# Kernel optimization log

Measured on AMD Instinct MI355X. Metric: run time of the kernel, lower is better.

Reference implementation:

```python
import jax, jax.numpy as jnp
import numpy as np

B, T, H, V, IN = 128, 1024, 512, 256, 1

def _uniform(key, shape, fan):
    bound = 1.0 / np.sqrt(fan)
    return jax.random.uniform(key, shape, jnp.float32, -bound, bound)

def setup_inputs() -> dict:
    key = jax.random.key(0)
    ks = jax.random.split(key, 11)
    return {
        'x': jax.random.normal(ks[0], (B, T), jnp.float32),
        # PyTorch LSTMCell params: weight_ih [4H, in], weight_hh [4H, H], biases [4H]
        'W_ih1': _uniform(ks[1], (4 * H, IN), H),
        'W_hh1': _uniform(ks[2], (4 * H, H), H),
        'b_ih1': _uniform(ks[3], (4 * H,), H),
        'b_hh1': _uniform(ks[4], (4 * H,), H),
        'W_ih2': _uniform(ks[5], (4 * H, H), H),
        'W_hh2': _uniform(ks[6], (4 * H, H), H),
        'b_ih2': _uniform(ks[7], (4 * H,), H),
        'b_hh2': _uniform(ks[8], (4 * H,), H),
        'W_lin': _uniform(ks[9], (V, H), H),
        'b_lin': _uniform(ks[10], (V,), H),
    }

def _lstm_cell(x, h, c, W_ih, W_hh, b_ih, b_hh):
    # gates in PyTorch order: input, forget, cell(g), output
    g = x @ W_ih.T + b_ih + h @ W_hh.T + b_hh  # [B, 4H]
    i, f, gg, o = jnp.split(g, 4, axis=-1)
    c_new = jax.nn.sigmoid(f) * c + jax.nn.sigmoid(i) * jnp.tanh(gg)
    h_new = jax.nn.sigmoid(o) * jnp.tanh(c_new)
    return h_new, c_new

def reference(x, W_ih1, W_hh1, b_ih1, b_hh1, W_ih2, W_hh2, b_ih2, b_hh2, W_lin, b_lin):
    Bb, Tt = x.shape
    Hh = W_hh1.shape[1]
    xt = x.T[:, :, None]  # [T, B, 1] -- each timestep is a [B,1] chunk

    def step(carry, x_t):
        h1, c1, h2, c2 = carry
        h1, c1 = _lstm_cell(x_t, h1, c1, W_ih1, W_hh1, b_ih1, b_hh1)
        h2, c2 = _lstm_cell(h1, h2, c2, W_ih2, W_hh2, b_ih2, b_hh2)
        return (h1, c1, h2, c2), h2

    z = jnp.zeros((Bb, Hh), x.dtype)
    _, h2_all = jax.lax.scan(step, (z, z, z, z), xt)  # h2_all: [T, B, H]
    # per-step linear + softmax is time-independent -> batch it after the scan
    logits = jnp.einsum('tbh,vh->btv', h2_all, W_lin) + b_lin  # [B, T, V]
    return jax.nn.softmax(logits, axis=-1)
```

## Files before the change

### kernel.cpp

```cpp
#include <hip/hip_runtime.h>
#include <hip/hip_bf16.h>

#define BB 128
#define TT 1024
#define HH 512
#define VV 256
#define NBLK 128

typedef __attribute__((ext_vector_type(8))) short short8;
typedef __attribute__((ext_vector_type(4))) float floatx4;

__device__ __forceinline__ floatx4 mfma16(short8 a, short8 b, floatx4 c) {
    return __builtin_amdgcn_mfma_f32_16x16x32_bf16(a, b, c, 0, 0, 0);
}
__device__ __forceinline__ float sigm(float x) { return 1.0f / (1.0f + __expf(-x)); }
__device__ __forceinline__ float tanh_fast(float x) {
    return 2.0f / (1.0f + __expf(-2.0f * x)) - 1.0f;
}
__device__ __forceinline__ void vmcnt0() {
    asm volatile("s_waitcnt vmcnt(0)" ::: "memory");
}
__device__ __forceinline__ void vm_fence() {
    asm volatile("s_waitcnt vmcnt(0)" ::: "memory");
    __builtin_amdgcn_sched_barrier(0);
}
__device__ __forceinline__ unsigned ald32(const unsigned* p) {
    return __hip_atomic_load(p, __ATOMIC_RELAXED, __HIP_MEMORY_SCOPE_AGENT);
}
__device__ __forceinline__ void ast32(unsigned* p, unsigned v) {
    __hip_atomic_store(p, v, __ATOMIC_RELAXED, __HIP_MEMORY_SCOPE_AGENT);
}
__device__ __forceinline__ short8 ld16_sc1(const __hip_bfloat16* p) {
    short8 v;
    asm volatile("global_load_dwordx4 %0, %1, off sc1" : "=v"(v) : "v"(p));
    return v;
}

__device__ __forceinline__ void poll1(const unsigned* line, unsigned tgt, int lane) {
    for (;;) {
        unsigned v = tgt;
        if (lane < 32) v = ald32(line + lane);
        if (__all((int)(v >= tgt))) return;
        __builtin_amdgcn_s_sleep(1);
    }
}
__device__ __forceinline__ void poll2(const unsigned* lineA, unsigned tA,
                                      const unsigned* lineB, unsigned tB, int lane) {
    const unsigned* p = (lane < 32) ? (lineA + lane) : (lineB + (lane - 32));
    const unsigned tgt = (lane < 32) ? tA : tB;
    for (;;) {
        unsigned v = ald32(p);
        if (__all((int)(v >= tgt))) return;
        __builtin_amdgcn_s_sleep(1);
    }
}

__global__ __launch_bounds__(256) void canon(
    const float* __restrict__ x,
    const float* __restrict__ Whh1, const float* __restrict__ Wih2,
    const float* __restrict__ Whh2, const float* __restrict__ Wlin,
    const float* __restrict__ bih1, const float* __restrict__ bhh1,
    const float* __restrict__ bih2, const float* __restrict__ bhh2,
    __hip_bfloat16* __restrict__ Whh1c, __hip_bfloat16* __restrict__ Wih2c,
    __hip_bfloat16* __restrict__ Whh2c, __hip_bfloat16* __restrict__ Wlinc,
    float* __restrict__ bsum1, float* __restrict__ bsum2,
    float* __restrict__ xT)
{
    const int tid = blockIdx.x * 256 + threadIdx.x;
    const int np  = gridDim.x * 256;
    for (int i = tid; i < 2048 * 512; i += np) {
        Whh1c[i] = __float2bfloat16(Whh1[i]);
        Wih2c[i] = __float2bfloat16(Wih2[i]);
        Whh2c[i] = __float2bfloat16(Whh2[i]);
    }
    for (int i = tid; i < 256 * 512; i += np) Wlinc[i] = __float2bfloat16(Wlin[i]);
    for (int i = tid; i < 2048; i += np) {
        bsum1[i] = bih1[i] + bhh1[i];
        bsum2[i] = bih2[i] + bhh2[i];
    }
    for (int i = tid; i < BB * TT; i += np) {
        int b = i >> 10, t = i & 1023;
        xT[t * BB + b] = x[i];
    }
}

__global__ __launch_bounds__(256, 1) void lstm_persist(
    const float* __restrict__ xT,
    const float* __restrict__ Wih1,
    const __hip_bfloat16* __restrict__ Whh1c,
    const float* __restrict__ bsum1,
    const __hip_bfloat16* __restrict__ Wih2c,
    const __hip_bfloat16* __restrict__ Whh2c,
    const float* __restrict__ bsum2,
    unsigned* __restrict__ flags,
    unsigned* __restrict__ h2ring,
    unsigned* __restrict__ h1all,
    __hip_bfloat16* __restrict__ h2slots)
{
    extern __shared__ __hip_bfloat16 lds[];

    const int bid   = blockIdx.x;
    const int stage = bid >> 6;
    const int half  = (bid >> 5) & 1;
    const int lb    = bid & 31;
    const int j0    = lb * 16;
    const int b0    = half * 64;
    const int w     = threadIdx.x >> 6;
    const int lane  = threadIdx.x & 63;
    const int q     = lane >> 4, ln = lane & 15;
    const int r0    = b0 + w * 16;

    unsigned* myflag       = flags + (stage * 2 + half) * 1024 + lb;
    const unsigned* line1  = flags + half * 1024;
    const unsigned* line2  = flags + (2 + half) * 1024;

    {
        const __hip_bfloat16* S0 = (stage == 0) ? Whh1c : Wih2c;
        for (int idx = threadIdx.x; idx < 4096; idx += 256) {
            const int g = idx >> 10, kk = (idx >> 6) & 15, l = idx & 63;
            const int lnt = l & 15, qt = l >> 4;
            const size_t src = (size_t)(g * 512 + j0 + lnt) * 512 + kk * 32 + qt * 8;
            *(float4*)(lds + idx * 8) = *(const float4*)(S0 + src);
            if (stage == 1)
                *(float4*)(lds + 32768 + idx * 8) = *(const float4*)(Whh2c + src);
        }
    }
    __syncthreads();

    float wv[4], bs[4];
    #pragma unroll
    for (int g = 0; g < 4; ++g) {
        const int j = g * 512 + j0 + ln;
        if (stage == 0) { wv[g] = Wih1[j]; bs[g] = bsum1[j]; }
        else            { wv[g] = 0.0f;    bs[g] = bsum2[j]; }
    }
    float cre[4] = {0.0f, 0.0f, 0.0f, 0.0f};

    const __hip_bfloat16* h1bf = (const __hip_bfloat16*)h1all;
    const int aoff = (r0 + ln) * HH + q * 8;
    const int jc   = j0 + (ln & ~1);
    const int rA   = (ln & 1) ? 2 : 0;
    const int bA   = r0 + q * 4 + rA;

    for (int t = 0; t < TT; ++t) {
        floatx4 acc[4];
        #pragma unroll
        for (int g = 0; g < 4; ++g) acc[g] = floatx4{0, 0, 0, 0};
        unsigned pk[4];

        if (stage == 0) {
            if (w == 0 && t > 0) poll1(line1, (unsigned)t, lane);
            __syncthreads();
            const __hip_bfloat16* hA = h1bf + (size_t)t * 65536;
            float4 xv4 = *(const float4*)(xT + t * BB + r0 + q * 4);
            short8 A0[16];
            #pragma unroll
            for (int kk = 0; kk < 16; ++kk)
                A0[kk] = *(const short8*)(hA + aoff + kk * 32);
            #pragma unroll
            for (int kk = 0; kk < 16; ++kk) {
                #pragma unroll
                for (int g = 0; g < 4; ++g)
                    acc[g] = mfma16(A0[kk],
                        *(const short8*)(lds + ((g * 16 + kk) * 64 + lane) * 8), acc[g]);
            }
            #pragma unroll
            for (int reg = 0; reg < 4; ++reg) {
                const float xv = ((const float*)&xv4)[reg];
                float gi = acc[0][reg] + xv * wv[0] + bs[0];
                float gf = acc[1][reg] + xv * wv[1] + bs[1];
                float gg = acc[2][reg] + xv * wv[2] + bs[2];
                float go = acc[3][reg] + xv * wv[3] + bs[3];
                float cn = sigm(gf) * cre[reg] + sigm(gi) * tanh_fast(gg);
                cre[reg] = cn;
                float hn = sigm(go) * tanh_fast(cn);
                __hip_bfloat16 hb = __float2bfloat16(hn);
                unsigned short us; __builtin_memcpy(&us, &hb, 2);
                unsigned mine = us;
                unsigned other = (unsigned)__shfl_xor((int)mine, 1, 64);
                pk[reg] = (ln & 1) ? ((other & 0xffffu) | (mine << 16))
                                   : ((mine & 0xffffu) | (other << 16));
            }
            unsigned* dst = h1all + (size_t)(t + 1) * 32768;
            ast32(dst + ((bA * HH + jc) >> 1),       pk[rA]);
            ast32(dst + (((bA + 1) * HH + jc) >> 1), pk[rA + 1]);
        } else {
            if (w == 0) poll2(line1, (unsigned)(t + 1), line2, (unsigned)t, lane);
            __syncthreads();
            const __hip_bfloat16* hB =
                (const __hip_bfloat16*)h2ring + (size_t)(t & 3) * 65536;
            short8 A1[16];
            #pragma unroll
            for (int kk = 0; kk < 16; ++kk) A1[kk] = ld16_sc1(hB + aoff + kk * 32);
            const __hip_bfloat16* hA = h1bf + (size_t)(t + 1) * 65536;
            short8 A0[16];
            #pragma unroll
            for (int kk = 0; kk < 16; ++kk)
                A0[kk] = *(const short8*)(hA + aoff + kk * 32);
            vm_fence();
            #pragma unroll
            for (int kk = 0; kk < 16; ++kk) {
                #pragma unroll
                for (int g = 0; g < 4; ++g)
                    acc[g] = mfma16(A0[kk],
                        *(const short8*)(lds + ((g * 16 + kk) * 64 + lane) * 8), acc[g]);
            }
            #pragma unroll
            for (int kk = 0; kk < 16; ++kk) {
                #pragma unroll
                for (int g = 0; g < 4; ++g)
                    acc[g] = mfma16(A1[kk],
                        *(const short8*)(lds + 32768 + ((g * 16 + kk) * 64 + lane) * 8), acc[g]);
            }
            #pragma unroll
            for (int reg = 0; reg < 4; ++reg) {
                float gi = acc[0][reg] + bs[0];
                float gf = acc[1][reg] + bs[1];
                float gg = acc[2][reg] + bs[2];
                float go = acc[3][reg] + bs[3];
                float cn = sigm(gf) * cre[reg] + sigm(gi) * tanh_fast(gg);
                cre[reg] = cn;
                float hn = sigm(go) * tanh_fast(cn);
                __hip_bfloat16 hb = __float2bfloat16(hn);
                unsigned short us; __builtin_memcpy(&us, &hb, 2);
                unsigned mine = us;
                unsigned other = (unsigned)__shfl_xor((int)mine, 1, 64);
                pk[reg] = (ln & 1) ? ((other & 0xffffu) | (mine << 16))
                                   : ((mine & 0xffffu) | (other << 16));
            }
            unsigned* dst = h2ring + (size_t)((t + 1) & 3) * 32768;
            ast32(dst + ((bA * HH + jc) >> 1),       pk[rA]);
            ast32(dst + (((bA + 1) * HH + jc) >> 1), pk[rA + 1]);
            unsigned* outs = (unsigned*)h2slots;
            outs[(((size_t)bA * TT + t) * HH + jc) >> 1]       = pk[rA];
            outs[(((size_t)(bA + 1) * TT + t) * HH + jc) >> 1] = pk[rA + 1];
        }

        vmcnt0();
        __syncthreads();
        if (threadIdx.x == 0) ast32(myflag, (unsigned)(t + 1));
    }
}

__global__ __launch_bounds__(256) void lin_softmax(
    const __hip_bfloat16* __restrict__ Wlinc,
    const float* __restrict__ blin,
    float* out)
{
    const __hip_bfloat16* slots = (const __hip_bfloat16*)out;
    const int w = threadIdx.x >> 6;
    const int lane = threadIdx.x & 63;
    const int q = lane >> 4, ln = lane & 15;
    const int r0 = blockIdx.x * 64 + w * 16;

    floatx4 acc[16];
    #pragma unroll
    for (int n = 0; n < 16; ++n) acc[n] = floatx4{0, 0, 0, 0};

    const size_t arow = (size_t)(r0 + ln) * HH + q * 8;
    #pragma unroll 4
    for (int kk = 0; kk < 16; ++kk) {
        short8 a = *(const short8*)(slots + arow + kk * 32);
        #pragma unroll
        for (int n = 0; n < 16; ++n) {
            short8 bf = *(const short8*)(Wlinc + (n * 16 + ln) * HH + kk * 32 + q * 8);
            acc[n] = mfma16(a, bf, acc[n]);
        }
    }

    float bl[16];
    #pragma unroll
    for (int n = 0; n < 16; ++n) bl[n] = blin[n * 16 + ln];

    #pragma unroll
    for (int reg = 0; reg < 4; ++reg) {
        float v[16];
        float mx = -3.4e38f;
        #pragma unroll
        for (int n = 0; n < 16; ++n) {
            v[n] = acc[n][reg] + bl[n];
            mx = fmaxf(mx, v[n]);
        }
        #pragma unroll
        for (int m = 1; m < 16; m <<= 1) mx = fmaxf(mx, __shfl_xor(mx, m));
        float sum = 0.0f;
        #pragma unroll
        for (int n = 0; n < 16; ++n) { v[n] = __expf(v[n] - mx); sum += v[n]; }
        #pragma unroll
        for (int m = 1; m < 16; m <<= 1) sum += __shfl_xor(sum, m);
        const float inv = 1.0f / sum;

        const int r = r0 + q * 4 + reg;
        #pragma unroll
        for (int n = 0; n < 16; ++n)
            out[(size_t)r * VV + n * 16 + ln] = v[n] * inv;
    }
}

extern "C" void kernel_launch(void* const* d_in, const int* in_sizes, int n_in,
                              void* d_out, int out_size, void* d_ws, size_t ws_size,
                              hipStream_t stream)
{
    const float* x     = (const float*)d_in[0];
    const float* W_ih1 = (const float*)d_in[1];
    const float* W_hh1 = (const float*)d_in[2];
    const float* b_ih1 = (const float*)d_in[3];
    const float* b_hh1 = (const float*)d_in[4];
    const float* W_ih2 = (const float*)d_in[5];
    const float* W_hh2 = (const float*)d_in[6];
    const float* b_ih2 = (const float*)d_in[7];
    const float* b_hh2 = (const float*)d_in[8];
    const float* W_lin = (const float*)d_in[9];
    const float* b_lin = (const float*)d_in[10];

    char* p = (char*)d_ws;
    unsigned* flags  = (unsigned*)p;   p += 16384;
    unsigned* h2ring = (unsigned*)p;   p += (size_t)4 * 131072;
    unsigned* h1all  = (unsigned*)p;   p += (size_t)1025 * 131072;
    const size_t zbytes = 16384 + (size_t)4 * 131072 + 131072;
    float* bsum1 = (float*)p;          p += 2048 * 4;
    float* bsum2 = (float*)p;          p += 2048 * 4;
    float* xT    = (float*)p;          p += (size_t)BB * TT * 4;
    __hip_bfloat16* Whh1c = (__hip_bfloat16*)p; p += (size_t)2048 * 512 * 2;
    __hip_bfloat16* Wih2c = (__hip_bfloat16*)p; p += (size_t)2048 * 512 * 2;
    __hip_bfloat16* Whh2c = (__hip_bfloat16*)p; p += (size_t)2048 * 512 * 2;
    __hip_bfloat16* Wlinc = (__hip_bfloat16*)p; p += (size_t)256 * 512 * 2;

    hipMemsetAsync(d_ws, 0, zbytes, stream);

    canon<<<dim3(512), dim3(256), 0, stream>>>(
        x, W_hh1, W_ih2, W_hh2, W_lin, b_ih1, b_hh1, b_ih2, b_hh2,
        Whh1c, Wih2c, Whh2c, Wlinc, bsum1, bsum2, xT);

    const int smem_bytes = 131072;
    (void)hipFuncSetAttribute((const void*)lstm_persist,
                              hipFuncAttributeMaxDynamicSharedMemorySize, smem_bytes);

    lstm_persist<<<dim3(NBLK), dim3(256), smem_bytes, stream>>>(
        xT, W_ih1, Whh1c, bsum1, Wih2c, Whh2c, bsum2,
        flags, h2ring, h1all, (__hip_bfloat16*)d_out);

    lin_softmax<<<dim3((TT * BB) / 64), dim3(256), 0, stream>>>(
        Wlinc, b_lin, (float*)d_out);
}
```

Measured before the change: 8.978 ms.

## Replace per-block flag polling with per-step atomic done counters and per-wave sync

Replaces the per-block flag lines, which wave 0 polled before a block-wide barrier, with one counter per timestep and half. Each block bumps its counter atomically once all four of its waves have finished, tracked through a small LDS counter ring. Every wave now polls a single counter on its own, and the end-of-step __syncthreads is gone, so waves can run ahead independently. Stage 1 also loads h1 before waiting on the h2 dependency, so that load overlaps the wait. In exchange it adds global atomics per step and leans on subtle memory ordering and reuse of the LDS counter ring.

```diff
diff --git a/kernel.cpp b/kernel.cpp
--- a/kernel.cpp
+++ b/kernel.cpp
@@ -35,23 +35,12 @@
     asm volatile("global_load_dwordx4 %0, %1, off sc1" : "=v"(v) : "v"(p));
     return v;
 }
-
-__device__ __forceinline__ void poll1(const unsigned* line, unsigned tgt, int lane) {
+__device__ __forceinline__ void pollc(const unsigned* c, unsigned tgt) {
+    int it = 0;
     for (;;) {
-        unsigned v = tgt;
-        if (lane < 32) v = ald32(line + lane);
-        if (__all((int)(v >= tgt))) return;
-        __builtin_amdgcn_s_sleep(1);
-    }
-}
-__device__ __forceinline__ void poll2(const unsigned* lineA, unsigned tA,
-                                      const unsigned* lineB, unsigned tB, int lane) {
-    const unsigned* p = (lane < 32) ? (lineA + lane) : (lineB + (lane - 32));
-    const unsigned tgt = (lane < 32) ? tA : tB;
-    for (;;) {
-        unsigned v = ald32(p);
-        if (__all((int)(v >= tgt))) return;
-        __builtin_amdgcn_s_sleep(1);
+        unsigned v = ald32(c);
+        if (v >= tgt) return;
+        if (++it > 64) __builtin_amdgcn_s_sleep(1);
     }
 }
 
@@ -92,12 +81,13 @@
     const __hip_bfloat16* __restrict__ Wih2c,
     const __hip_bfloat16* __restrict__ Whh2c,
     const float* __restrict__ bsum2,
-    unsigned* __restrict__ flags,
+    unsigned* __restrict__ done,
     unsigned* __restrict__ h2ring,
     unsigned* __restrict__ h1all,
     __hip_bfloat16* __restrict__ h2slots)
 {
     extern __shared__ __hip_bfloat16 lds[];
+    __shared__ unsigned cnt[16];
 
     const int bid   = blockIdx.x;
     const int stage = bid >> 6;
@@ -110,9 +100,9 @@
     const int q     = lane >> 4, ln = lane & 15;
     const int r0    = b0 + w * 16;
 
-    unsigned* myflag       = flags + (stage * 2 + half) * 1024 + lb;
-    const unsigned* line1  = flags + half * 1024;
-    const unsigned* line2  = flags + (2 + half) * 1024;
+    unsigned* done1h = done + half * 2048;
+    unsigned* done2h = done + 4096 + half * 2048;
+    unsigned* mydone = (stage == 0) ? done1h : done2h;
 
     {
         const __hip_bfloat16* S0 = (stage == 0) ? Whh1c : Wih2c;
@@ -125,6 +115,7 @@
                 *(float4*)(lds + 32768 + idx * 8) = *(const float4*)(Whh2c + src);
         }
     }
+    if (threadIdx.x < 16) cnt[threadIdx.x] = 0;
     __syncthreads();
 
     float wv[4], bs[4];
@@ -141,6 +132,8 @@
     const int jc   = j0 + (ln & ~1);
     const int rA   = (ln & 1) ? 2 : 0;
     const int bA   = r0 + q * 4 + rA;
+    const int o0   = (bA * HH + jc) >> 1;
+    const int o1   = ((bA + 1) * HH + jc) >> 1;
 
     for (int t = 0; t < TT; ++t) {
         floatx4 acc[4];
@@ -149,8 +142,8 @@
         unsigned pk[4];
 
         if (stage == 0) {
-            if (w == 0 && t > 0) poll1(line1, (unsigned)t, lane);
-            __syncthreads();
+            if (t > 0) pollc(done1h + (t - 1), 32u);
+            __builtin_amdgcn_sched_barrier(0);
             const __hip_bfloat16* hA = h1bf + (size_t)t * 65536;
             float4 xv4 = *(const float4*)(xT + t * BB + r0 + q * 4);
             short8 A0[16];
@@ -182,21 +175,31 @@
                                    : ((mine & 0xffffu) | (other << 16));
             }
             unsigned* dst = h1all + (size_t)(t + 1) * 32768;
-            ast32(dst + ((bA * HH + jc) >> 1),       pk[rA]);
-            ast32(dst + (((bA + 1) * HH + jc) >> 1), pk[rA + 1]);
+            ast32(dst + o0, pk[rA]);
+            ast32(dst + o1, pk[rA + 1]);
+            vmcnt0();
+            if (lane == 0) {
+                unsigned old = atomicAdd(&cnt[t & 15], 1u);
+                if (old == 3) {
+                    cnt[(t + 8) & 15] = 0;
+                    atomicAdd(mydone + t, 1u);
+                }
+            }
         } else {
-            if (w == 0) poll2(line1, (unsigned)(t + 1), line2, (unsigned)t, lane);
-            __syncthreads();
+            pollc(done1h + t, 32u);
+            __builtin_amdgcn_sched_barrier(0);
+            const __hip_bfloat16* hA = h1bf + (size_t)(t + 1) * 65536;
+            short8 A0[16];
+            #pragma unroll
+            for (int kk = 0; kk < 16; ++kk)
+                A0[kk] = *(const short8*)(hA + aoff + kk * 32);
+            if (t > 0) pollc(done2h + (t - 1), 32u);
+            __builtin_amdgcn_sched_barrier(0);
             const __hip_bfloat16* hB =
                 (const __hip_bfloat16*)h2ring + (size_t)(t & 3) * 65536;
             short8 A1[16];
             #pragma unroll
             for (int kk = 0; kk < 16; ++kk) A1[kk] = ld16_sc1(hB + aoff + kk * 32);
-            const __hip_bfloat16* hA = h1bf + (size_t)(t + 1) * 65536;
-            short8 A0[16];
-            #pragma unroll
-            for (int kk = 0; kk < 16; ++kk)
-                A0[kk] = *(const short8*)(hA + aoff + kk * 32);
             vm_fence();
             #pragma unroll
             for (int kk = 0; kk < 16; ++kk) {
@@ -229,16 +232,20 @@
                                    : ((mine & 0xffffu) | (other << 16));
             }
             unsigned* dst = h2ring + (size_t)((t + 1) & 3) * 32768;
-            ast32(dst + ((bA * HH + jc) >> 1),       pk[rA]);
-            ast32(dst + (((bA + 1) * HH + jc) >> 1), pk[rA + 1]);
+            ast32(dst + o0, pk[rA]);
+            ast32(dst + o1, pk[rA + 1]);
+            vmcnt0();
+            if (lane == 0) {
+                unsigned old = atomicAdd(&cnt[t & 15], 1u);
+                if (old == 3) {
+                    cnt[(t + 8) & 15] = 0;
+                    atomicAdd(mydone + t, 1u);
+                }
+            }
             unsigned* outs = (unsigned*)h2slots;
             outs[(((size_t)bA * TT + t) * HH + jc) >> 1]       = pk[rA];
             outs[(((size_t)(bA + 1) * TT + t) * HH + jc) >> 1] = pk[rA + 1];
         }
-
-        vmcnt0();
-        __syncthreads();
-        if (threadIdx.x == 0) ast32(myflag, (unsigned)(t + 1));
     }
 }
 
@@ -314,10 +321,10 @@
     const float* b_lin = (const float*)d_in[10];
 
     char* p = (char*)d_ws;
-    unsigned* flags  = (unsigned*)p;   p += 16384;
+    unsigned* done   = (unsigned*)p;   p += 32768;
     unsigned* h2ring = (unsigned*)p;   p += (size_t)4 * 131072;
     unsigned* h1all  = (unsigned*)p;   p += (size_t)1025 * 131072;
-    const size_t zbytes = 16384 + (size_t)4 * 131072 + 131072;
+    const size_t zbytes = 32768 + (size_t)4 * 131072 + 131072;
     float* bsum1 = (float*)p;          p += 2048 * 4;
     float* bsum2 = (float*)p;          p += 2048 * 4;
     float* xT    = (float*)p;          p += (size_t)BB * TT * 4;
@@ -338,7 +345,7 @@
 
     lstm_persist<<<dim3(NBLK), dim3(256), smem_bytes, stream>>>(
         xT, W_ih1, Whh1c, bsum1, Wih2c, Whh2c, bsum2,
-        flags, h2ring, h1all, (__hip_bfloat16*)d_out);
+        done, h2ring, h1all, (__hip_bfloat16*)d_out);
 
     lin_softmax<<<dim3((TT * BB) / 64), dim3(256), 0, stream>>>(
         Wlinc, b_lin, (float*)d_out);
```

Result: slower. 9.664 ms (+7.6%).

## Split stage-2 wait so h1 matmul overlaps the h2 recurrence dependency

Applied to the files above, without the earlier changes.

Stage-1 blocks publish their step flag (and a duplicate flag line) right after writing h1 instead of at the end of the step. Stage-2 blocks now wait only on the h1 flag, run the W_ih2 matmul, and only then wait for the h2 flag of the previous step before loading h2 and running the W_hh2 part. Stage 2 also sets its flag before the h2slots output stores. The goal is to shorten the critical path of the serial recurrence by overlapping the input-projection matmul with the wait on other blocks. The trade-off is more polling traffic, because every wave polls the duplicated flag line.

```diff
diff --git a/kernel.cpp b/kernel.cpp
--- a/kernel.cpp
+++ b/kernel.cpp
@@ -40,16 +40,6 @@
     for (;;) {
         unsigned v = tgt;
         if (lane < 32) v = ald32(line + lane);
-        if (__all((int)(v >= tgt))) return;
-        __builtin_amdgcn_s_sleep(1);
-    }
-}
-__device__ __forceinline__ void poll2(const unsigned* lineA, unsigned tA,
-                                      const unsigned* lineB, unsigned tB, int lane) {
-    const unsigned* p = (lane < 32) ? (lineA + lane) : (lineB + (lane - 32));
-    const unsigned tgt = (lane < 32) ? tA : tB;
-    for (;;) {
-        unsigned v = ald32(p);
         if (__all((int)(v >= tgt))) return;
         __builtin_amdgcn_s_sleep(1);
     }
@@ -93,8 +83,8 @@
     const __hip_bfloat16* __restrict__ Whh2c,
     const float* __restrict__ bsum2,
     unsigned* __restrict__ flags,
+    unsigned* __restrict__ h1all,
     unsigned* __restrict__ h2ring,
-    unsigned* __restrict__ h1all,
     __hip_bfloat16* __restrict__ h2slots)
 {
     extern __shared__ __hip_bfloat16 lds[];
@@ -110,9 +100,11 @@
     const int q     = lane >> 4, ln = lane & 15;
     const int r0    = b0 + w * 16;
 
-    unsigned* myflag       = flags + (stage * 2 + half) * 1024 + lb;
-    const unsigned* line1  = flags + half * 1024;
-    const unsigned* line2  = flags + (2 + half) * 1024;
+    unsigned* line1  = flags + half * 1024;
+    unsigned* line2  = flags + (2 + half) * 1024;
+    unsigned* line1c = flags + (4 + half) * 1024;
+    unsigned* myflag  = (stage == 0) ? (line1 + lb) : (line2 + lb);
+    unsigned* myflagc = line1c + lb;
 
     {
         const __hip_bfloat16* S0 = (stage == 0) ? Whh1c : Wih2c;
@@ -141,6 +133,8 @@
     const int jc   = j0 + (ln & ~1);
     const int rA   = (ln & 1) ? 2 : 0;
     const int bA   = r0 + q * 4 + rA;
+    const int o0   = (bA * HH + jc) >> 1;
+    const int o1   = ((bA + 1) * HH + jc) >> 1;
 
     for (int t = 0; t < TT; ++t) {
         floatx4 acc[4];
@@ -182,22 +176,22 @@
                                    : ((mine & 0xffffu) | (other << 16));
             }
             unsigned* dst = h1all + (size_t)(t + 1) * 32768;
-            ast32(dst + ((bA * HH + jc) >> 1),       pk[rA]);
-            ast32(dst + (((bA + 1) * HH + jc) >> 1), pk[rA + 1]);
+            ast32(dst + o0, pk[rA]);
+            ast32(dst + o1, pk[rA + 1]);
+            vmcnt0();
+            __syncthreads();
+            if (threadIdx.x == 0) {
+                ast32(myflag,  (unsigned)(t + 1));
+                ast32(myflagc, (unsigned)(t + 1));
+            }
         } else {
-            if (w == 0) poll2(line1, (unsigned)(t + 1), line2, (unsigned)t, lane);
-            __syncthreads();
-            const __hip_bfloat16* hB =
-                (const __hip_bfloat16*)h2ring + (size_t)(t & 3) * 65536;
-            short8 A1[16];
-            #pragma unroll
-            for (int kk = 0; kk < 16; ++kk) A1[kk] = ld16_sc1(hB + aoff + kk * 32);
+            poll1(line1c, (unsigned)(t + 1), lane);
+            asm volatile("" ::: "memory");
             const __hip_bfloat16* hA = h1bf + (size_t)(t + 1) * 65536;
             short8 A0[16];
             #pragma unroll
             for (int kk = 0; kk < 16; ++kk)
                 A0[kk] = *(const short8*)(hA + aoff + kk * 32);
-            vm_fence();
             #pragma unroll
             for (int kk = 0; kk < 16; ++kk) {
                 #pragma unroll
@@ -205,12 +199,22 @@
                     acc[g] = mfma16(A0[kk],
                         *(const short8*)(lds + ((g * 16 + kk) * 64 + lane) * 8), acc[g]);
             }
-            #pragma unroll
-            for (int kk = 0; kk < 16; ++kk) {
+            if (w == 0 && t > 0) poll1(line2, (unsigned)t, lane);
+            __syncthreads();
+            if (t > 0) {
+                const __hip_bfloat16* hB =
+                    (const __hip_bfloat16*)h2ring + (size_t)(t & 3) * 65536;
+                short8 A1[16];
                 #pragma unroll
-                for (int g = 0; g < 4; ++g)
-                    acc[g] = mfma16(A1[kk],
-                        *(const short8*)(lds + 32768 + ((g * 16 + kk) * 64 + lane) * 8), acc[g]);
+                for (int kk = 0; kk < 16; ++kk) A1[kk] = ld16_sc1(hB + aoff + kk * 32);
+                vm_fence();
+                #pragma unroll
+                for (int kk = 0; kk < 16; ++kk) {
+                    #pragma unroll
+                    for (int g = 0; g < 4; ++g)
+                        acc[g] = mfma16(A1[kk],
+                            *(const short8*)(lds + 32768 + ((g * 16 + kk) * 64 + lane) * 8), acc[g]);
+                }
             }
             #pragma unroll
             for (int reg = 0; reg < 4; ++reg) {
@@ -229,16 +233,15 @@
                                    : ((mine & 0xffffu) | (other << 16));
             }
             unsigned* dst = h2ring + (size_t)((t + 1) & 3) * 32768;
-            ast32(dst + ((bA * HH + jc) >> 1),       pk[rA]);
-            ast32(dst + (((bA + 1) * HH + jc) >> 1), pk[rA + 1]);
+            ast32(dst + o0, pk[rA]);
+            ast32(dst + o1, pk[rA + 1]);
+            vmcnt0();
+            __syncthreads();
+            if (threadIdx.x == 0) ast32(myflag, (unsigned)(t + 1));
             unsigned* outs = (unsigned*)h2slots;
             outs[(((size_t)bA * TT + t) * HH + jc) >> 1]       = pk[rA];
             outs[(((size_t)(bA + 1) * TT + t) * HH + jc) >> 1] = pk[rA + 1];
         }
-
-        vmcnt0();
-        __syncthreads();
-        if (threadIdx.x == 0) ast32(myflag, (unsigned)(t + 1));
     }
 }
 
@@ -314,10 +317,10 @@
     const float* b_lin = (const float*)d_in[10];
 
     char* p = (char*)d_ws;
-    unsigned* flags  = (unsigned*)p;   p += 16384;
+    unsigned* flags  = (unsigned*)p;   p += 24576;
+    unsigned* h1all  = (unsigned*)p;   p += (size_t)1025 * 131072;
+    const size_t zbytes = 24576 + 131072;
     unsigned* h2ring = (unsigned*)p;   p += (size_t)4 * 131072;
-    unsigned* h1all  = (unsigned*)p;   p += (size_t)1025 * 131072;
-    const size_t zbytes = 16384 + (size_t)4 * 131072 + 131072;
     float* bsum1 = (float*)p;          p += 2048 * 4;
     float* bsum2 = (float*)p;          p += 2048 * 4;
     float* xT    = (float*)p;          p += (size_t)BB * TT * 4;
@@ -338,7 +341,7 @@
 
     lstm_persist<<<dim3(NBLK), dim3(256), smem_bytes, stream>>>(
         xT, W_ih1, Whh1c, bsum1, Wih2c, Whh2c, bsum2,
-        flags, h2ring, h1all, (__hip_bfloat16*)d_out);
+        flags, h1all, h2ring, (__hip_bfloat16*)d_out);
 
     lin_softmax<<<dim3((TT * BB) / 64), dim3(256), 0, stream>>>(
         Wlinc, b_lin, (float*)d_out);
```

New measurement: 8.560 ms. 4.7% less time.
